# Kernel optimization log

Hardware: AMD Instinct MI355X
Metric: run time of the kernel (lower is better)

Reference implementation:

```python
import jax, jax.numpy as jnp
import numpy as np

B, C, H, W = 4, 256, 64, 64
CH = C // 2


def setup_inputs() -> dict:
    key = jax.random.key(0)
    ks = jax.random.split(key, 8)
    s_in = 1.0 / np.sqrt(C)  # conv2d default init scale (fan_in = C for 1x1)
    return {
        "a": jax.random.normal(ks[0], (B, C, H, W), dtype=jnp.float32),
        "p": jax.random.normal(ks[1], (B, C, H, W), dtype=jnp.float32),
        "Wq": jax.random.uniform(ks[2], (CH, C), jnp.float32, -s_in, s_in),
        "bq": jax.random.uniform(ks[3], (CH,), jnp.float32, -s_in, s_in),
        "Wk": jax.random.uniform(ks[4], (CH, C), jnp.float32, -s_in, s_in),
        "bk": jax.random.uniform(ks[5], (CH,), jnp.float32, -s_in, s_in),
        "Wv": jax.random.uniform(ks[6], (C, C), jnp.float32, -s_in, s_in),
        "bv": jax.random.uniform(ks[7], (C,), jnp.float32, -s_in, s_in),
    }


def reference(a, p, Wq, bq, Wk, bk, Wv, bv):
    b, c, h, w = a.shape
    hw = h * w
    # 1x1 convs == per-pixel channel matmuls; flatten spatial dims to hw
    Q = jnp.einsum('oc,bchw->bohw', Wq, a).reshape(b, -1, hw) + bq[None, :, None]   # [B, C/2, HW]
    K = jnp.einsum('oc,bchw->bohw', Wk, p).reshape(b, -1, hw) + bk[None, :, None]   # [B, C/2, HW]
    V = jnp.einsum('oc,bchw->bohw', Wv, p).reshape(b, -1, hw) + bv[None, :, None]   # [B, C,   HW]
    # attn[b,m,n] = softmax_n( Q[:, :, m] . K[:, :, n] )
    attn = jax.nn.softmax(jnp.einsum('bcm,bcn->bmn', Q, K), axis=-1)                # [B, HW, HW]
    # out[b,c,m] = sum_n V[b,c,n] * attn[b,m,n]  (V @ attn^T)
    out = jnp.einsum('bcn,bmn->bcm', V, attn).reshape(b, c, h, w)
    return out + a
```

## Files before the change

kernel.cpp:

```cpp
#include <hip/hip_runtime.h>
#include <stdint.h>

#define B_ 4
#define C_ 256
#define CH_ 128
#define HW_ 4096
#define L2E 1.44269504f
#define SHIFT_L2 14.4269504f

typedef __bf16 bf16;
typedef __bf16 v8bf __attribute__((ext_vector_type(8)));
typedef __bf16 v4bf __attribute__((ext_vector_type(4)));
typedef float v4f __attribute__((ext_vector_type(4)));

#define GAS __attribute__((address_space(1)))
#define LAS __attribute__((address_space(3)))

__device__ __forceinline__ void async_copy16(const void* gptr, void* lptr) {
  __builtin_amdgcn_global_load_lds((GAS void*)gptr, (LAS void*)lptr, 16, 0, 0);
}

__global__ __launch_bounds__(512)
void proj_kernel(const float* __restrict__ a, const float* __restrict__ p,
                 const float* __restrict__ Wq, const float* __restrict__ bq,
                 const float* __restrict__ Wk, const float* __restrict__ bk,
                 const float* __restrict__ Wv, const float* __restrict__ bv,
                 bf16* __restrict__ Qt, bf16* __restrict__ Kt, bf16* __restrict__ Vn)
{
  __shared__ bf16 Xt[64 * 266];
  __shared__ bf16 Ds[9600];

  const int t = threadIdx.x;
  const int lane = t & 63;
  const int w = t >> 6;
  const int l15 = lane & 15;
  const int q = lane >> 4;

  const int s0 = blockIdx.x * 64;
  const int b = blockIdx.y;
  const int z = blockIdx.z;

  const float* X; const float* W; const float* bias;
  if (z == 0)      { X = a; W = Wq; bias = bq; }
  else if (z == 1) { X = p; W = Wk; bias = bk; }
  else             { X = p; W = Wv + (size_t)(z - 2) * 128 * C_; bias = bv + (z - 2) * 128; }

  const float* Xb = X + ((size_t)b * C_) * HW_;
  for (int j = 0; j < 16; ++j) {
    int linear = t + 512 * j;
    int s = linear & 63;
    int cp = linear >> 6;
    float x0 = Xb[(size_t)(2 * cp) * HW_ + s0 + s];
    float x1 = Xb[(size_t)(2 * cp + 1) * HW_ + s0 + s];
    unsigned short u0 = __builtin_bit_cast(unsigned short, (bf16)x0);
    unsigned short u1 = __builtin_bit_cast(unsigned short, (bf16)x1);
    *(unsigned int*)&Xt[s * 266 + 2 * cp] = (unsigned int)u0 | ((unsigned int)u1 << 16);
  }

  v8bf Af[8];
  const float* Wrow = W + (size_t)(16 * w + l15) * C_;
  #pragma unroll
  for (int kk = 0; kk < 8; ++kk) {
    v8bf f;
    #pragma unroll
    for (int j = 0; j < 8; ++j) f[j] = (bf16)Wrow[kk * 32 + q * 8 + j];
    Af[kk] = f;
  }

  __syncthreads();

  v4f acc[4];
  #pragma unroll
  for (int ns = 0; ns < 4; ++ns) { v4f zz = {0.f, 0.f, 0.f, 0.f}; acc[ns] = zz; }

  #pragma unroll
  for (int ns = 0; ns < 4; ++ns)
    #pragma unroll
    for (int kk = 0; kk < 8; ++kk) {
      v8bf Bf = *(const v8bf*)&Xt[(16 * ns + l15) * 266 + kk * 32 + q * 8];
      acc[ns] = __builtin_amdgcn_mfma_f32_16x16x32_bf16(Af[kk], Bf, acc[ns], 0, 0, 0);
    }

  if (z < 2) {
    #pragma unroll
    for (int ns = 0; ns < 4; ++ns)
      #pragma unroll
      for (int r = 0; r < 4; ++r)
        Ds[(16 * ns + l15) * 150 + 16 * w + 4 * q + r] =
            (bf16)(acc[ns][r] + bias[16 * w + 4 * q + r]);
    __syncthreads();
    bf16* dst = (z == 0) ? Qt : Kt;
    #pragma unroll
    for (int i = 0; i < 2; ++i) {
      int idx = t + 512 * i;
      int s = idx >> 4, ch = (idx & 15) * 8;
      *(v8bf*)&dst[((size_t)b * HW_ + s0 + s) * CH_ + ch] = *(const v8bf*)&Ds[s * 150 + ch];
    }
  } else {
    int o0 = (z - 2) * 128;
    #pragma unroll
    for (int ns = 0; ns < 4; ++ns)
      #pragma unroll
      for (int r = 0; r < 4; ++r)
        Ds[(16 * w + 4 * q + r) * 72 + l15 * 4 + ns] =
            (bf16)(acc[ns][r] + bias[16 * w + 4 * q + r]);
    __syncthreads();
    #pragma unroll
    for (int i = 0; i < 2; ++i) {
      int idx = t + 512 * i;
      int o = idx >> 3, ch = (idx & 7) * 8;
      *(v8bf*)&Vn[((size_t)b * C_ + o0 + o) * HW_ + s0 + ch] = *(const v8bf*)&Ds[o * 72 + ch];
    }
  }
}

#define LDS_V 16640
#define LDS_P 49920
#define LDS_TOTAL 68352

__global__ __launch_bounds__(256, 2)
void attn_kernel(const bf16* __restrict__ Qt, const bf16* __restrict__ Kt,
                 const bf16* __restrict__ Vn, const float* __restrict__ a,
                 float* __restrict__ out, bf16* __restrict__ Op,
                 float* __restrict__ Ls, int nsplit)
{
  extern __shared__ char smem[];
  const int t = threadIdx.x;
  const int lane = t & 63;
  const int w = t >> 6;
  const int l15 = lane & 15;
  const int q = lane >> 4;
  const int b = blockIdx.y;
  const int sp = blockIdx.z;
  const int m0 = blockIdx.x * 128;

  v8bf Qf[2][4];
  #pragma unroll
  for (int s = 0; s < 2; ++s) {
    const bf16* qrow = Qt + ((size_t)b * HW_ + m0 + 32 * w + 16 * s + l15) * CH_;
    #pragma unroll
    for (int kk = 0; kk < 4; ++kk)
      Qf[s][kk] = *(const v8bf*)&qrow[kk * 32 + q * 8];
  }

  v4f O[2][16];
  #pragma unroll
  for (int s = 0; s < 2; ++s)
    #pragma unroll
    for (int cs = 0; cs < 16; ++cs) { v4f zz = {0.f, 0.f, 0.f, 0.f}; O[s][cs] = zz; }
  float lsum[2][4];
  #pragma unroll
  for (int s = 0; s < 2; ++s)
    #pragma unroll
    for (int r = 0; r < 4; ++r) lsum[s][r] = 0.f;

  const bf16* Kb = Kt + (size_t)b * HW_ * CH_;
  const bf16* Vb = Vn + (size_t)b * C_ * HW_;
  char* Pbase = smem + LDS_P + w * 4608;

  const int NT = 64 / nsplit;
  const int t0 = sp * NT;

  for (int nt = 0; nt < NT; ++nt) {
    int n0 = (t0 + nt) * 64;

    #pragma unroll
    for (int j = 0; j < 4; ++j) {
      int i = 4 * j + w;
      async_copy16(Kb + ((size_t)(n0 + i + 16 * q)) * CH_ + l15 * 8, smem + i * 1040);
    }
    #pragma unroll
    for (int j = 0; j < 8; ++j) {
      int i = 4 * j + w;
      async_copy16(Vb + ((size_t)(i + 32 * (lane >> 3))) * HW_ + n0 + (lane & 7) * 8,
                   smem + LDS_V + i * 1040);
    }
    __syncthreads();

    v4f S[2][4];
    #pragma unroll
    for (int s = 0; s < 2; ++s)
      #pragma unroll
      for (int sub = 0; sub < 4; ++sub) { v4f zz = {0.f, 0.f, 0.f, 0.f}; S[s][sub] = zz; }
    #pragma unroll
    for (int sub = 0; sub < 4; ++sub)
      #pragma unroll
      for (int kk = 0; kk < 4; ++kk) {
        v8bf Kf = *(const v8bf*)(smem + l15 * 1040 + sub * 256 + kk * 64 + q * 16);
        S[0][sub] = __builtin_amdgcn_mfma_f32_16x16x32_bf16(Qf[0][kk], Kf, S[0][sub], 0, 0, 0);
        S[1][sub] = __builtin_amdgcn_mfma_f32_16x16x32_bf16(Qf[1][kk], Kf, S[1][sub], 0, 0, 0);
      }

    #pragma unroll
    for (int s = 0; s < 2; ++s)
      #pragma unroll
      for (int r = 0; r < 4; ++r) {
        v4bf pp;
        float p0 = exp2f(S[s][0][r] * L2E - SHIFT_L2);
        float p1 = exp2f(S[s][1][r] * L2E - SHIFT_L2);
        float p2 = exp2f(S[s][2][r] * L2E - SHIFT_L2);
        float p3 = exp2f(S[s][3][r] * L2E - SHIFT_L2);
        pp[0] = (bf16)p0; pp[1] = (bf16)p1; pp[2] = (bf16)p2; pp[3] = (bf16)p3;
        lsum[s][r] += (p0 + p1) + (p2 + p3);
        *(v4bf*)(Pbase + (16 * s + 4 * q + r) * 144 + l15 * 8) = pp;
      }

    v8bf Pf[2][2];
    #pragma unroll
    for (int s = 0; s < 2; ++s)
      #pragma unroll
      for (int kk = 0; kk < 2; ++kk)
        Pf[s][kk] = *(const v8bf*)(Pbase + (16 * s + l15) * 144 + kk * 64 + q * 16);

    #pragma unroll
    for (int cs = 0; cs < 16; ++cs)
      #pragma unroll
      for (int kk = 0; kk < 2; ++kk) {
        v8bf Vf = *(const v8bf*)(smem + LDS_V +
                                 (16 * (cs & 1) + l15) * 1040 + (cs >> 1) * 128 + kk * 64 + q * 16);
        O[0][cs] = __builtin_amdgcn_mfma_f32_16x16x32_bf16(Pf[0][kk], Vf, O[0][cs], 0, 0, 0);
        O[1][cs] = __builtin_amdgcn_mfma_f32_16x16x32_bf16(Pf[1][kk], Vf, O[1][cs], 0, 0, 0);
      }

    __syncthreads();
  }

  float lfin[2][4];
  #pragma unroll
  for (int s = 0; s < 2; ++s)
    #pragma unroll
    for (int r = 0; r < 4; ++r) {
      float l = lsum[s][r];
      l += __shfl_xor(l, 1);
      l += __shfl_xor(l, 2);
      l += __shfl_xor(l, 4);
      l += __shfl_xor(l, 8);
      lfin[s][r] = l;
    }

  if (nsplit > 1 && l15 == 0) {
    #pragma unroll
    for (int s = 0; s < 2; ++s)
      #pragma unroll
      for (int r = 0; r < 4; ++r) {
        int m = m0 + 32 * w + 16 * s + 4 * q + r;
        Ls[((size_t)sp * B_ + b) * HW_ + m] = lfin[s][r];
      }
  }

  bf16* T = (bf16*)smem;
  float linv[2][4];
  #pragma unroll
  for (int s = 0; s < 2; ++s)
    #pragma unroll
    for (int r = 0; r < 4; ++r) linv[s][r] = (nsplit == 1) ? 1.0f / lfin[s][r] : 1.0f;

  for (int round = 0; round < 2; ++round) {
    __syncthreads();
    if ((w >> 1) == round) {
      bf16* Tw = T + (w & 1) * 12288;
      #pragma unroll
      for (int s = 0; s < 2; ++s)
        #pragma unroll
        for (int cs = 0; cs < 16; ++cs)
          #pragma unroll
          for (int r = 0; r < 4; ++r)
            Tw[(16 * cs + l15) * 48 + 16 * s + 4 * q + r] = (bf16)(O[s][cs][r] * linv[s][r]);
    }
    __syncthreads();
    #pragma unroll
    for (int it = 0; it < 8; ++it) {
      int idx = t + 256 * it;
      int tt = idx >> 10;
      int c = (idx >> 2) & 255;
      int mc = idx & 3;
      int wavew = round * 2 + tt;
      int mg = m0 + 32 * wavew + mc * 8;
      v8bf val = *(const v8bf*)&T[tt * 12288 + c * 48 + mc * 8];
      if (nsplit == 1) {
        size_t gi = ((size_t)b * C_ + c) * HW_ + mg;
        #pragma unroll
        for (int j2 = 0; j2 < 8; ++j2) out[gi + j2] = (float)val[j2] + a[gi + j2];
      } else {
        size_t gi = (((size_t)sp * B_ + b) * C_ + c) * HW_ + mg;
        *(v8bf*)&Op[gi] = val;
      }
    }
  }
}

__global__ __launch_bounds__(256)
void combine_kernel(const bf16* __restrict__ Op, const float* __restrict__ Ls,
                    const float* __restrict__ a, float* __restrict__ out, int nsplit)
{
  int idx = blockIdx.x * 256 + threadIdx.x;
  int m8 = (idx & (HW_ / 8 - 1)) * 8;
  int bc = idx >> 9;
  int b = bc >> 8;

  float acc[8], L[8];
  #pragma unroll
  for (int j = 0; j < 8; ++j) { acc[j] = 0.f; L[j] = 0.f; }
  for (int s = 0; s < nsplit; ++s) {
    v8bf o = *(const v8bf*)&Op[((size_t)s * B_ * C_ + bc) * HW_ + m8];
    const float* lp = Ls + ((size_t)s * B_ + b) * HW_ + m8;
    #pragma unroll
    for (int j = 0; j < 8; ++j) { acc[j] += (float)o[j]; L[j] += lp[j]; }
  }
  const float* ap = a + (size_t)bc * HW_ + m8;
  float* op = out + (size_t)bc * HW_ + m8;
  #pragma unroll
  for (int j = 0; j < 8; ++j) op[j] = acc[j] / L[j] + ap[j];
}

extern "C" void kernel_launch(void* const* d_in, const int* in_sizes, int n_in,
                              void* d_out, int out_size, void* d_ws, size_t ws_size,
                              hipStream_t stream) {
  const float* a  = (const float*)d_in[0];
  const float* p  = (const float*)d_in[1];
  const float* Wq = (const float*)d_in[2];
  const float* bq = (const float*)d_in[3];
  const float* Wk = (const float*)d_in[4];
  const float* bk = (const float*)d_in[5];
  const float* Wv = (const float*)d_in[6];
  const float* bv = (const float*)d_in[7];
  float* out = (float*)d_out;

  bf16* Qt = (bf16*)d_ws;
  bf16* Kt = Qt + (size_t)B_ * HW_ * CH_;
  bf16* Vn = Kt + (size_t)B_ * HW_ * CH_;

  const size_t proj_bytes = 16777216ull;
  const size_t part_bytes = (size_t)B_ * C_ * HW_ * 2;
  const size_t stat_bytes = (size_t)B_ * HW_ * 4;
  auto need = [&](int S) { return proj_bytes + (size_t)S * (part_bytes + stat_bytes); };

  int S;
  if      (ws_size >= need(4)) S = 4;
  else if (ws_size >= need(2)) S = 2;
  else                         S = 1;

  bf16* Op = (bf16*)((char*)d_ws + proj_bytes);
  float* Ls = (float*)((char*)d_ws + proj_bytes + (size_t)S * part_bytes);

  dim3 pg(HW_ / 64, B_, 4);
  proj_kernel<<<pg, 512, 0, stream>>>(a, p, Wq, bq, Wk, bk, Wv, bv, Qt, Kt, Vn);

  hipFuncSetAttribute(reinterpret_cast<const void*>(&attn_kernel),
                      hipFuncAttributeMaxDynamicSharedMemorySize, LDS_TOTAL);
  dim3 ag(HW_ / 128, B_, S);
  attn_kernel<<<ag, 256, LDS_TOTAL, stream>>>(Qt, Kt, Vn, a, out, Op, Ls, S);

  if (S > 1) {
    int nblk = (B_ * C_ * HW_ / 8) / 256;
    combine_kernel<<<nblk, 256, 0, stream>>>(Op, Ls, a, out, S);
  }
}
```

Before: 179.1 us.

## Prefetch next K/V tiles during attention compute; merge V projection halves per block

```diff
diff --git a/kernel.cpp b/kernel.cpp
--- a/kernel.cpp
+++ b/kernel.cpp
@@ -12,6 +12,7 @@
 typedef __bf16 v8bf __attribute__((ext_vector_type(8)));
 typedef __bf16 v4bf __attribute__((ext_vector_type(4)));
 typedef float v4f __attribute__((ext_vector_type(4)));
+struct f4 { float x, y, z, w; };
 
 #define GAS __attribute__((address_space(1)))
 #define LAS __attribute__((address_space(3)))
@@ -40,10 +41,10 @@
   const int b = blockIdx.y;
   const int z = blockIdx.z;
 
-  const float* X; const float* W; const float* bias;
-  if (z == 0)      { X = a; W = Wq; bias = bq; }
-  else if (z == 1) { X = p; W = Wk; bias = bk; }
-  else             { X = p; W = Wv + (size_t)(z - 2) * 128 * C_; bias = bv + (z - 2) * 128; }
+  const float* X    = (z == 0) ? a  : p;
+  const float* W    = (z == 0) ? Wq : (z == 1 ? Wk : Wv);
+  const float* bias = (z == 0) ? bq : (z == 1 ? bk : bv);
+  const int nh = (z == 2) ? 2 : 1;
 
   const float* Xb = X + ((size_t)b * C_) * HW_;
   for (int j = 0; j < 16; ++j) {
@@ -56,60 +57,62 @@
     unsigned short u1 = __builtin_bit_cast(unsigned short, (bf16)x1);
     *(unsigned int*)&Xt[s * 266 + 2 * cp] = (unsigned int)u0 | ((unsigned int)u1 << 16);
   }
-
-  v8bf Af[8];
-  const float* Wrow = W + (size_t)(16 * w + l15) * C_;
-  #pragma unroll
-  for (int kk = 0; kk < 8; ++kk) {
-    v8bf f;
-    #pragma unroll
-    for (int j = 0; j < 8; ++j) f[j] = (bf16)Wrow[kk * 32 + q * 8 + j];
-    Af[kk] = f;
-  }
-
   __syncthreads();
 
-  v4f acc[4];
-  #pragma unroll
-  for (int ns = 0; ns < 4; ++ns) { v4f zz = {0.f, 0.f, 0.f, 0.f}; acc[ns] = zz; }
-
-  #pragma unroll
-  for (int ns = 0; ns < 4; ++ns)
+  for (int h = 0; h < nh; ++h) {
+    v8bf Af[8];
+    const float* Wrow = W + (size_t)(h * 128 + 16 * w + l15) * C_;
     #pragma unroll
     for (int kk = 0; kk < 8; ++kk) {
-      v8bf Bf = *(const v8bf*)&Xt[(16 * ns + l15) * 266 + kk * 32 + q * 8];
-      acc[ns] = __builtin_amdgcn_mfma_f32_16x16x32_bf16(Af[kk], Bf, acc[ns], 0, 0, 0);
-    }
-
-  if (z < 2) {
+      f4 f0 = *(const f4*)&Wrow[kk * 32 + q * 8];
+      f4 f1 = *(const f4*)&Wrow[kk * 32 + q * 8 + 4];
+      v8bf f;
+      f[0] = (bf16)f0.x; f[1] = (bf16)f0.y; f[2] = (bf16)f0.z; f[3] = (bf16)f0.w;
+      f[4] = (bf16)f1.x; f[5] = (bf16)f1.y; f[6] = (bf16)f1.z; f[7] = (bf16)f1.w;
+      Af[kk] = f;
+    }
+
+    v4f acc[4];
+    #pragma unroll
+    for (int ns = 0; ns < 4; ++ns) { v4f zz = {0.f, 0.f, 0.f, 0.f}; acc[ns] = zz; }
     #pragma unroll
     for (int ns = 0; ns < 4; ++ns)
       #pragma unroll
-      for (int r = 0; r < 4; ++r)
-        Ds[(16 * ns + l15) * 150 + 16 * w + 4 * q + r] =
-            (bf16)(acc[ns][r] + bias[16 * w + 4 * q + r]);
-    __syncthreads();
-    bf16* dst = (z == 0) ? Qt : Kt;
-    #pragma unroll
-    for (int i = 0; i < 2; ++i) {
-      int idx = t + 512 * i;
-      int s = idx >> 4, ch = (idx & 15) * 8;
-      *(v8bf*)&dst[((size_t)b * HW_ + s0 + s) * CH_ + ch] = *(const v8bf*)&Ds[s * 150 + ch];
-    }
-  } else {
-    int o0 = (z - 2) * 128;
-    #pragma unroll
-    for (int ns = 0; ns < 4; ++ns)
-      #pragma unroll
-      for (int r = 0; r < 4; ++r)
-        Ds[(16 * w + 4 * q + r) * 72 + l15 * 4 + ns] =
-            (bf16)(acc[ns][r] + bias[16 * w + 4 * q + r]);
-    __syncthreads();
-    #pragma unroll
-    for (int i = 0; i < 2; ++i) {
-      int idx = t + 512 * i;
-      int o = idx >> 3, ch = (idx & 7) * 8;
-      *(v8bf*)&Vn[((size_t)b * C_ + o0 + o) * HW_ + s0 + ch] = *(const v8bf*)&Ds[o * 72 + ch];
+      for (int kk = 0; kk < 8; ++kk) {
+        v8bf Bf = *(const v8bf*)&Xt[(16 * ns + l15) * 266 + kk * 32 + q * 8];
+        acc[ns] = __builtin_amdgcn_mfma_f32_16x16x32_bf16(Af[kk], Bf, acc[ns], 0, 0, 0);
+      }
+
+    if (z < 2) {
+      #pragma unroll
+      for (int ns = 0; ns < 4; ++ns)
+        #pragma unroll
+        for (int r = 0; r < 4; ++r)
+          Ds[(16 * ns + l15) * 150 + 16 * w + 4 * q + r] =
+              (bf16)(acc[ns][r] + bias[16 * w + 4 * q + r]);
+      __syncthreads();
+      bf16* dst = (z == 0) ? Qt : Kt;
+      #pragma unroll
+      for (int i = 0; i < 2; ++i) {
+        int idx = t + 512 * i;
+        int s = idx >> 4, ch = (idx & 15) * 8;
+        *(v8bf*)&dst[((size_t)b * HW_ + s0 + s) * CH_ + ch] = *(const v8bf*)&Ds[s * 150 + ch];
+      }
+    } else {
+      #pragma unroll
+      for (int ns = 0; ns < 4; ++ns)
+        #pragma unroll
+        for (int r = 0; r < 4; ++r)
+          Ds[(16 * w + 4 * q + r) * 72 + l15 * 4 + ns] =
+              (bf16)(acc[ns][r] + bias[h * 128 + 16 * w + 4 * q + r]);
+      __syncthreads();
+      #pragma unroll
+      for (int i = 0; i < 2; ++i) {
+        int idx = t + 512 * i;
+        int o = idx >> 3, ch = (idx & 7) * 8;
+        *(v8bf*)&Vn[((size_t)b * C_ + h * 128 + o) * HW_ + s0 + ch] = *(const v8bf*)&Ds[o * 72 + ch];
+      }
+      if (h == 0) __syncthreads();
     }
   }
 }
@@ -161,21 +164,28 @@
   const int NT = 64 / nsplit;
   const int t0 = sp * NT;
 
-  for (int nt = 0; nt < NT; ++nt) {
-    int n0 = (t0 + nt) * 64;
-
+  auto stageK = [&](int n0) {
     #pragma unroll
     for (int j = 0; j < 4; ++j) {
       int i = 4 * j + w;
       async_copy16(Kb + ((size_t)(n0 + i + 16 * q)) * CH_ + l15 * 8, smem + i * 1040);
     }
+  };
+  auto stageV = [&](int n0) {
     #pragma unroll
     for (int j = 0; j < 8; ++j) {
       int i = 4 * j + w;
       async_copy16(Vb + ((size_t)(i + 32 * (lane >> 3))) * HW_ + n0 + (lane & 7) * 8,
                    smem + LDS_V + i * 1040);
     }
-    __syncthreads();
+  };
+
+  stageK(t0 * 64);
+  stageV(t0 * 64);
+  __syncthreads();
+
+  for (int nt = 0; nt < NT; ++nt) {
+    int n0 = (t0 + nt) * 64;
 
     v4f S[2][4];
     #pragma unroll
@@ -190,6 +200,9 @@
         S[0][sub] = __builtin_amdgcn_mfma_f32_16x16x32_bf16(Qf[0][kk], Kf, S[0][sub], 0, 0, 0);
         S[1][sub] = __builtin_amdgcn_mfma_f32_16x16x32_bf16(Qf[1][kk], Kf, S[1][sub], 0, 0, 0);
       }
+
+    __syncthreads();
+    if (nt + 1 < NT) stageK(n0 + 64);
 
     #pragma unroll
     for (int s = 0; s < 2; ++s)
@@ -223,6 +236,7 @@
       }
 
     __syncthreads();
+    if (nt + 1 < NT) stageV(n0 + 64);
   }
 
   float lfin[2][4];
@@ -343,7 +357,7 @@
   bf16* Op = (bf16*)((char*)d_ws + proj_bytes);
   float* Ls = (float*)((char*)d_ws + proj_bytes + (size_t)S * part_bytes);
 
-  dim3 pg(HW_ / 64, B_, 4);
+  dim3 pg(HW_ / 64, B_, 3);
   proj_kernel<<<pg, 512, 0, stream>>>(a, p, Wq, bq, Wk, bk, Wv, bv, Qt, Kt, Vn);
 
   hipFuncSetAttribute(reinterpret_cast<const void*>(&attn_kernel),
```

New measurement: 186.2 us. 4.0% more time.
